# Performance work log

Hardware: AMD Instinct MI355X
Metric: run time of the kernel (lower is better)

## Reference

```python
import jax, jax.numpy as jnp
import numpy as np

C = 32          # d_model / channels
D_STATE = 32
D_CONV = 4
EXPAND = 2
D_INNER = EXPAND * C          # 64
DT_RANK = (C + 15) // 16      # ceil(32/16) = 2
EPS = 1e-5


def _conv2d(x, w, b):
    # x: (B,C,H,W), w: (O,I,3,3), stride 1, padding 1 (torch Conv2d)
    y = jax.lax.conv_general_dilated(
        x, w, window_strides=(1, 1), padding=[(1, 1), (1, 1)],
        dimension_numbers=("NCHW", "OIHW", "NCHW"))
    return y + b[None, :, None, None]


def _silu(x):
    return x * jax.nn.sigmoid(x)


def _mamba(xs, in_proj_w, conv1d_w, conv1d_b, x_proj_w, dt_proj_w, dt_proj_b,
           A_log, Dp, out_proj_w):
    # xs: (B, L, C)
    xz = xs @ in_proj_w.T                       # (B, L, 2*D_INNER)
    xm, z = jnp.split(xz, 2, axis=-1)           # each (B, L, D_INNER)

    # causal depthwise conv1d along L (torch: padding=d_conv-1 then [..., :L])
    xc = xm.transpose(0, 2, 1)                  # (B, D_INNER, L)
    xc = jax.lax.conv_general_dilated(
        xc, conv1d_w, window_strides=(1,), padding=[(D_CONV - 1, 0)],
        dimension_numbers=("NCH", "OIH", "NCH"),
        feature_group_count=D_INNER)
    xm = _silu((xc + conv1d_b[None, :, None]).transpose(0, 2, 1))  # (B,L,D_INNER)

    x_dbl = xm @ x_proj_w.T                     # (B, L, DT_RANK + 2*D_STATE)
    dt = x_dbl[..., :DT_RANK]
    Bm = x_dbl[..., DT_RANK:DT_RANK + D_STATE]  # (B, L, N)
    Cm = x_dbl[..., DT_RANK + D_STATE:]         # (B, L, N)

    delta = jax.nn.softplus(dt @ dt_proj_w.T + dt_proj_b)  # (B, L, D_INNER)
    A = -jnp.exp(A_log)                                     # (D_INNER, N)

    deltaA = jnp.exp(delta[..., None] * A)                           # (B,L,D,N)
    deltaBx = delta[..., None] * Bm[:, :, None, :] * xm[..., None]   # (B,L,D,N)

    def combine(c1, c2):
        a1, b1 = c1
        a2, b2 = c2
        return a1 * a2, a2 * b1 + b2

    # parallel linear recurrence h_t = deltaA_t * h_{t-1} + deltaBx_t
    _, hstate = jax.lax.associative_scan(combine, (deltaA, deltaBx), axis=1)

    y = jnp.einsum("bldn,bln->bld", hstate, Cm) + xm * Dp
    y = y * _silu(z)
    return y @ out_proj_w.T                     # (B, L, C)


def setup_inputs() -> dict:
    key = jax.random.key(0)
    ks = jax.random.split(key, 16)
    s = 0.02
    inp = {
        "x": jax.random.normal(ks[0], (4, C, 64, 64), dtype=jnp.float32),
        "conv1_w": jax.random.normal(ks[1], (2 * C, C, 3, 3), jnp.float32) * s,
        "conv1_b": jnp.zeros((2 * C,), jnp.float32),
        "conv2_w": jax.random.normal(ks[2], (C, 2 * C, 3, 3), jnp.float32) * s,
        "conv2_b": jnp.zeros((C,), jnp.float32),
        "ln_g": jnp.ones((C,), jnp.float32),
        "ln_b": jnp.zeros((C,), jnp.float32),
        "in_proj_w": jax.random.normal(ks[3], (2 * D_INNER, C), jnp.float32) * s,
        "conv1d_w": jax.random.normal(ks[4], (D_INNER, 1, D_CONV), jnp.float32) * 0.1,
        "conv1d_b": jnp.zeros((D_INNER,), jnp.float32),
        "x_proj_w": jax.random.normal(ks[5], (DT_RANK + 2 * D_STATE, D_INNER), jnp.float32) * s,
        "dt_proj_w": jax.random.normal(ks[6], (D_INNER, DT_RANK), jnp.float32) * 0.1,
        "dt_proj_b": jax.random.normal(ks[7], (D_INNER,), jnp.float32) * 0.1 - 4.0,
        "A_log": jnp.log(jnp.tile(jnp.arange(1, D_STATE + 1, dtype=jnp.float32), (D_INNER, 1))),
        "Dp": jnp.ones((D_INNER,), jnp.float32),
        "out_proj_w": jax.random.normal(ks[8], (C, D_INNER), jnp.float32) * s,
        "smooth_w": jax.random.normal(ks[9], (C, C, 3, 3), jnp.float32) * s,
        "smooth_b": jnp.zeros((C,), jnp.float32),
    }
    return inp


def reference(x, conv1_w, conv1_b, conv2_w, conv2_b, ln_g, ln_b,
              in_proj_w, conv1d_w, conv1d_b, x_proj_w, dt_proj_w, dt_proj_b,
              A_log, Dp, out_proj_w, smooth_w, smooth_b):
    b, c, h, w = x.shape
    # convb residual
    t = jax.nn.relu(_conv2d(x, conv1_w, conv1_b))
    x = _conv2d(t, conv2_w, conv2_b) + x
    # reshape (b,c,h,w) -> (b, h*w, c) row-major (faithful to torch .reshape)
    xs = x.reshape(b, -1, c)
    # LayerNorm over last dim
    mu = jnp.mean(xs, axis=-1, keepdims=True)
    var = jnp.mean(jnp.square(xs - mu), axis=-1, keepdims=True)
    xs = (xs - mu) * jax.lax.rsqrt(var + EPS) * ln_g + ln_b
    # Mamba block
    y = _mamba(xs, in_proj_w, conv1d_w, conv1d_b, x_proj_w, dt_proj_w,
               dt_proj_b, A_log, Dp, out_proj_w)
    y = y.transpose(0, 2, 1).reshape(b, c, h, w)
    return _conv2d(y, smooth_w, smooth_b)
```

## Files before the change

### kernel.cpp

```cpp
#include <hip/hip_runtime.h>
#include <math.h>

#define SEQL 4096
#define L2E 1.44269504088896340736f

#if defined(__has_builtin)
#if __has_builtin(__builtin_amdgcn_exp2f)
#define FAST_EXP2(x) __builtin_amdgcn_exp2f(x)
#endif
#endif
#ifndef FAST_EXP2
#define FAST_EXP2(x) exp2f(x)
#endif

__device__ __forceinline__ float sigmoid_f(float x){ return 1.0f/(1.0f+expf(-x)); }

template<int CI, int CO, int COG, bool RELU, bool RES>
__global__ __launch_bounds__(256) void conv3x3_k(const float* __restrict__ in,
    const float* __restrict__ wgt, const float* __restrict__ bias,
    const float* __restrict__ res, float* __restrict__ out)
{
  constexpr int CIT = CI/4;
  __shared__ float tin[4][2][6][72];
  __shared__ float red[3][4][COG][66];
  const int tid  = threadIdx.x;
  const int lane = tid & 63;
  const int ty   = tid >> 6;
  const int h0   = blockIdx.x * 4;
  const int co0  = blockIdx.y * COG;
  const int b    = blockIdx.z;

  if (lane < 24){
    int cl = lane / 12, rem = lane % 12, r = rem >> 1, side = rem & 1;
    tin[ty][cl][r][side ? 68 : 3] = 0.0f;
  }

  float acc[4][COG];
  #pragma unroll
  for (int rr=0;rr<4;++rr)
    #pragma unroll
    for (int u=0;u<COG;++u) acc[rr][u] = 0.0f;

  const int ci0 = ty*CIT;
  for (int cig = ci0; cig < ci0 + CIT; cig += 2){
    #pragma unroll
    for (int k=0;k<3;++k){
      int idx4 = lane + (k<<6);
      int row  = idx4 >> 4;
      int cl = row/6, r = row - cl*6;
      int w4 = (idx4 & 15) << 2;
      int h  = h0 - 1 + r;
      float4 v = make_float4(0.f,0.f,0.f,0.f);
      if (h>=0 && h<64)
        v = *(const float4*)(in + ((size_t)(b*CI+cig+cl)*64 + h)*64 + w4);
      *(float4*)&tin[ty][cl][r][4+w4] = v;
    }
    #pragma unroll
    for (int cl=0; cl<2; ++cl){
      float rv[6][3];
      #pragma unroll
      for (int r=0;r<6;++r)
        #pragma unroll
        for (int c=0;c<3;++c)
          rv[r][c] = tin[ty][cl][r][3+lane+c];
      #pragma unroll
      for (int u=0;u<COG;++u){
        const float* wp = wgt + ((size_t)(co0+u)*CI + cig + cl)*9;
        #pragma unroll
        for (int rr=0;rr<4;++rr)
          #pragma unroll
          for (int j=0;j<3;++j){
            acc[rr][u] = fmaf(rv[rr+j][0], wp[3*j+0], acc[rr][u]);
            acc[rr][u] = fmaf(rv[rr+j][1], wp[3*j+1], acc[rr][u]);
            acc[rr][u] = fmaf(rv[rr+j][2], wp[3*j+2], acc[rr][u]);
          }
      }
    }
  }
  if (ty > 0){
    #pragma unroll
    for (int rr=0;rr<4;++rr)
      #pragma unroll
      for (int u=0;u<COG;++u) red[ty-1][rr][u][lane] = acc[rr][u];
  }
  __syncthreads();
  if (ty == 0){
    #pragma unroll
    for (int rr=0;rr<4;++rr)
      #pragma unroll
      for (int u=0;u<COG;++u){
        float s = acc[rr][u] + red[0][rr][u][lane] + red[1][rr][u][lane]
                + red[2][rr][u][lane] + bias[co0+u];
        size_t ob = ((size_t)(b*CO+co0+u)*64 + h0+rr)*64 + lane;
        if constexpr (RES)  s += res[ob];
        if constexpr (RELU) s = fmaxf(s, 0.0f);
        out[ob] = s;
      }
  }
}

__global__ __launch_bounds__(512) void mamba_in_k(const float* __restrict__ x2,
    const float* __restrict__ g, const float* __restrict__ be,
    const float* __restrict__ Wip, const float* __restrict__ cw,
    const float* __restrict__ cb, const float* __restrict__ Wxp,
    const float* __restrict__ Wdt, const float* __restrict__ bdt,
    const float* __restrict__ A_log,
    float* __restrict__ xm2, float* __restrict__ szb, float* __restrict__ dlt,
    float* __restrict__ Bm, float* __restrict__ Cm,
    float* __restrict__ cA, float* __restrict__ cH)
{
  __shared__ float xn[35][37];
  __shared__ float xm[64][36];
  __shared__ float xt[32][67];
  __shared__ float xd[32][67];
  const int tid = threadIdx.x;
  const int bi = blockIdx.x >> 7;
  const int chunk = blockIdx.x & 127;
  const int l0 = chunk << 5;

  if (tid < 35){
    int tok = l0 - 3 + tid;
    if (tok >= 0){
      const float* row = x2 + (size_t)bi*131072 + (size_t)tok*32;
      float v[32];
      #pragma unroll
      for (int c=0;c<32;c+=4){
        float4 f = *(const float4*)(row + c);
        v[c]=f.x; v[c+1]=f.y; v[c+2]=f.z; v[c+3]=f.w;
      }
      float p[8];
      #pragma unroll
      for (int j2=0;j2<8;++j2) p[j2]=v[j2];
      #pragma unroll
      for (int i=8;i<32;i+=8){
        #pragma unroll
        for (int j2=0;j2<8;++j2) p[j2]+=v[i+j2];
      }
      float mu = (((p[0]+p[1])+(p[2]+p[3]))+((p[4]+p[5])+(p[6]+p[7]))) * 0.03125f;
      float q[8];
      #pragma unroll
      for (int j2=0;j2<8;++j2){ float dd=v[j2]-mu; q[j2]=dd*dd; }
      #pragma unroll
      for (int i=8;i<32;i+=8){
        #pragma unroll
        for (int j2=0;j2<8;++j2){ float dd=v[i+j2]-mu; q[j2]+=dd*dd; }
      }
      float var = (((q[0]+q[1])+(q[2]+q[3]))+((q[4]+q[5])+(q[6]+q[7]))) * 0.03125f;
      float rstd = 1.0f / sqrtf(var + 1e-5f);
      #pragma unroll
      for (int c=0;c<32;++c) xn[tid][c] = (v[c]-mu)*rstd*g[c] + be[c];
    } else {
      #pragma unroll
      for (int c=0;c<32;++c) xn[tid][c] = 0.0f;
    }
  }
  __syncthreads();

  {
    const int t = tid & 31, jg = tid >> 5;
    float xv[32];
    #pragma unroll
    for (int c=0;c<32;++c) xv[c] = xn[t+3][c];
    #pragma unroll
    for (int k=0;k<8;++k){
      int j = jg*8 + k;
      const float* wr = Wip + j*32;
      float a = 0.0f;
      #pragma unroll
      for (int c=0;c<32;++c) a = fmaf(xv[c], wr[c], a);
      if (j < 64) xm[j][t+3] = a;
      else        szb[((size_t)(bi*64 + (j-64)))*SEQL + l0 + t] = a * sigmoid_f(a);
    }
  }
  if (tid < 192){
    int t = tid % 3, j = tid / 3;
    float xv[32];
    #pragma unroll
    for (int c=0;c<32;++c) xv[c] = xn[t][c];
    const float* wr = Wip + j*32;
    float a = 0.0f;
    #pragma unroll
    for (int c=0;c<32;++c) a = fmaf(xv[c], wr[c], a);
    xm[j][t] = a;
  }
  __syncthreads();

  {
    const int d = tid >> 3, t0 = (tid & 7) << 2;
    const float w0=cw[d*4], w1=cw[d*4+1], w2=cw[d*4+2], w3=cw[d*4+3], bv=cb[d];
    float r[4];
    #pragma unroll
    for (int k=0;k<4;++k){
      int t = t0 + k;
      float a = xm[d][t]*w0 + xm[d][t+1]*w1 + xm[d][t+2]*w2 + xm[d][t+3]*w3 + bv;
      float s = a * sigmoid_f(a);
      xt[t][d] = s;
      r[k] = s;
    }
    *(float4*)(xm2 + ((size_t)(bi*64+d))*SEQL + l0 + t0) = make_float4(r[0],r[1],r[2],r[3]);
  }
  __syncthreads();

  {
    const int tok = tid & 31, jg = tid >> 5;
    float xv[64];
    #pragma unroll
    for (int c=0;c<64;++c) xv[c] = xt[tok][c];
    for (int j=jg; j<66; j+=16){
      const float* wr = Wxp + j*64;
      float a = 0.0f;
      #pragma unroll
      for (int c=0;c<64;++c) a = fmaf(xv[c], wr[c], a);
      xd[tok][j] = a;
    }
  }
  __syncthreads();

  {
    const int tok = tid & 31, gg = tid >> 5;
    float dt0 = xd[tok][0], dt1 = xd[tok][1];
    #pragma unroll
    for (int k=0;k<4;++k){
      int d2 = gg*4 + k;
      float v = dt0*Wdt[d2*2] + dt1*Wdt[d2*2+1] + bdt[d2];
      float sp = fmaxf(v,0.0f) + log1pf(expf(-fabsf(v)));
      dlt[((size_t)(bi*64+d2))*SEQL + l0 + tok] = sp;
      xm[d2][tok] = sp;
    }
    const int which = gg >> 3, n0 = (gg & 7)*4;
    float* dst = which ? Cm : Bm;
    const int s0 = 2 + which*32 + n0;
    float4 f;
    f.x = xd[tok][s0]; f.y = xd[tok][s0+1]; f.z = xd[tok][s0+2]; f.w = xd[tok][s0+3];
    *(float4*)(dst + ((size_t)bi*SEQL + l0 + tok)*32 + n0) = f;
  }
  __syncthreads();

  {
    const int d  = tid >> 3;
    const int gg = tid & 7;
    const int bd = bi*64 + d;
    float Av2[4], h[4] = {0,0,0,0}, aP[4] = {1,1,1,1};
    #pragma unroll
    for (int j=0;j<4;++j) Av2[j] = -expf(A_log[d*32 + gg + 8*j]) * L2E;
    #pragma unroll 4
    for (int t=0;t<32;++t){
      float dlv = xm[d][t];
      float xv2 = xt[t][d];
      #pragma unroll
      for (int j=0;j<4;++j){
        float bv = xd[t][2 + gg + 8*j];
        float a = FAST_EXP2(dlv*Av2[j]);
        h[j] = fmaf(a, h[j], dlv*bv*xv2);
        aP[j] *= a;
      }
    }
    #pragma unroll
    for (int j=0;j<4;++j){
      size_t idx = (((size_t)bd<<5) + gg + 8*j)*128 + chunk;
      cA[idx] = aP[j]; cH[idx] = h[j];
    }
  }
}

__global__ __launch_bounds__(256) void scan_p2(const float* __restrict__ dlt,
    const float* __restrict__ xssm, const float* __restrict__ Bm,
    const float* __restrict__ Cm, const float* __restrict__ A_log,
    const float* __restrict__ Dp, const float* __restrict__ sz,
    const float* __restrict__ cA, const float* __restrict__ cHs,
    float* __restrict__ yt)
{
  __shared__ float pre[32][9];
  const int tid = threadIdx.x;
  const int n = tid & 31;
  const int grp = blockIdx.x & 15;
  const int chunk = grp*8 + (tid >> 5);
  const int bd = blockIdx.x >> 4;
  const int b = bd >> 6, d = bd & 63;
  const int l0 = chunk << 5;

  if (tid < 32){
    const float* pa = cA  + (((size_t)bd<<5)+tid)*128;
    const float* ph = cHs + (((size_t)bd<<5)+tid)*128;
    float hrun = 0.0f;
    for (int c=0;c<grp*8;c+=4){
      float4 a4 = *(const float4*)(pa+c);
      float4 h4 = *(const float4*)(ph+c);
      hrun = fmaf(a4.x,hrun,h4.x);
      hrun = fmaf(a4.y,hrun,h4.y);
      hrun = fmaf(a4.z,hrun,h4.z);
      hrun = fmaf(a4.w,hrun,h4.w);
    }
    int c = grp*8;
    float4 a4 = *(const float4*)(pa+c);
    float4 h4 = *(const float4*)(ph+c);
    pre[tid][0]=hrun; hrun=fmaf(a4.x,hrun,h4.x);
    pre[tid][1]=hrun; hrun=fmaf(a4.y,hrun,h4.y);
    pre[tid][2]=hrun; hrun=fmaf(a4.z,hrun,h4.z);
    pre[tid][3]=hrun; hrun=fmaf(a4.w,hrun,h4.w);
    a4 = *(const float4*)(pa+c+4);
    h4 = *(const float4*)(ph+c+4);
    pre[tid][4]=hrun; hrun=fmaf(a4.x,hrun,h4.x);
    pre[tid][5]=hrun; hrun=fmaf(a4.y,hrun,h4.y);
    pre[tid][6]=hrun; hrun=fmaf(a4.z,hrun,h4.z);
    pre[tid][7]=hrun;
  }
  __syncthreads();

  const float Av2 = -expf(A_log[d*32+n]) * L2E;
  const float Dv = Dp[d];
  const float* del = dlt  + (size_t)bd*SEQL + l0;
  const float* xp  = xssm + (size_t)bd*SEQL + l0;
  const float* szp = sz   + (size_t)bd*SEQL + l0;
  const float* Bp  = Bm + ((size_t)b*SEQL + l0)*32 + n;
  const float* Cp  = Cm + ((size_t)b*SEQL + l0)*32 + n;
  float* yp = yt + (size_t)bd*SEQL + l0;
  float h = pre[n][tid >> 5];
  #pragma unroll 2
  for (int i0=0;i0<32;i0+=4){
    float4 d4 = *(const float4*)(del+i0);
    float4 x4 = *(const float4*)(xp +i0);
    float4 s4 = *(const float4*)(szp+i0);
    float b0 = Bp[(i0+0)*32], b1 = Bp[(i0+1)*32], b2 = Bp[(i0+2)*32], b3 = Bp[(i0+3)*32];
    float c0 = Cp[(i0+0)*32], c1 = Cp[(i0+1)*32], c2 = Cp[(i0+2)*32], c3 = Cp[(i0+3)*32];
    float a0 = FAST_EXP2(d4.x*Av2); h = fmaf(a0,h, d4.x*b0*x4.x);
    float v0 = h*c0;
    float a1 = FAST_EXP2(d4.y*Av2); h = fmaf(a1,h, d4.y*b1*x4.y);
    float v1 = h*c1;
    float a2 = FAST_EXP2(d4.z*Av2); h = fmaf(a2,h, d4.z*b2*x4.z);
    float v2 = h*c2;
    float a3 = FAST_EXP2(d4.w*Av2); h = fmaf(a3,h, d4.w*b3*x4.w);
    float v3 = h*c3;
    v0 += __shfl_xor(v0,16); v0 += __shfl_xor(v0,8); v0 += __shfl_xor(v0,4);
    v0 += __shfl_xor(v0,2);  v0 += __shfl_xor(v0,1);
    v1 += __shfl_xor(v1,16); v1 += __shfl_xor(v1,8); v1 += __shfl_xor(v1,4);
    v1 += __shfl_xor(v1,2);  v1 += __shfl_xor(v1,1);
    v2 += __shfl_xor(v2,16); v2 += __shfl_xor(v2,8); v2 += __shfl_xor(v2,4);
    v2 += __shfl_xor(v2,2);  v2 += __shfl_xor(v2,1);
    v3 += __shfl_xor(v3,16); v3 += __shfl_xor(v3,8); v3 += __shfl_xor(v3,4);
    v3 += __shfl_xor(v3,2);  v3 += __shfl_xor(v3,1);
    if (n==0){
      yp[i0+0] = fmaf(x4.x, Dv, v0) * s4.x;
      yp[i0+1] = fmaf(x4.y, Dv, v1) * s4.y;
      yp[i0+2] = fmaf(x4.z, Dv, v2) * s4.z;
      yp[i0+3] = fmaf(x4.w, Dv, v3) * s4.w;
    }
  }
}

__global__ __launch_bounds__(512) void outproj_k(const float* __restrict__ yt,
    const float* __restrict__ Wout, float* __restrict__ ym)
{
  __shared__ float ys[64][67];
  const int tid = threadIdx.x, lane = tid & 63, ty = tid >> 6;
  const int bi = blockIdx.x >> 6;
  const int l0 = (blockIdx.x & 63) << 6;
  for (int r=ty; r<64; r+=8)
    ys[lane][r] = yt[((size_t)(bi*64+r))*SEQL + l0 + lane];
  __syncthreads();
  float yv[64];
  #pragma unroll
  for (int c=0;c<64;++c) yv[c] = ys[lane][c];
  #pragma unroll
  for (int jj=0;jj<4;++jj){
    int j = ty*4 + jj;
    const float* wr = Wout + j*64;
    float acc = 0.0f;
    #pragma unroll
    for (int c=0;c<64;++c) acc = fmaf(yv[c], wr[c], acc);
    ym[((size_t)(bi*32+j))*SEQL + l0 + lane] = acc;
  }
}

extern "C" void kernel_launch(void* const* d_in, const int* in_sizes, int n_in,
                              void* d_out, int out_size, void* d_ws, size_t ws_size,
                              hipStream_t stream) {
  const float* x        = (const float*)d_in[0];
  const float* conv1_w  = (const float*)d_in[1];
  const float* conv1_b  = (const float*)d_in[2];
  const float* conv2_w  = (const float*)d_in[3];
  const float* conv2_b  = (const float*)d_in[4];
  const float* ln_g     = (const float*)d_in[5];
  const float* ln_b     = (const float*)d_in[6];
  const float* in_proj_w= (const float*)d_in[7];
  const float* conv1d_w = (const float*)d_in[8];
  const float* conv1d_b = (const float*)d_in[9];
  const float* x_proj_w = (const float*)d_in[10];
  const float* dt_proj_w= (const float*)d_in[11];
  const float* dt_proj_b= (const float*)d_in[12];
  const float* A_log    = (const float*)d_in[13];
  const float* Dp       = (const float*)d_in[14];
  const float* out_proj_w=(const float*)d_in[15];
  const float* smooth_w = (const float*)d_in[16];
  const float* smooth_b = (const float*)d_in[17];
  float* out = (float*)d_out;

  float* ws = (float*)d_ws;
  float* t      = ws;
  float* x2     = t      + 1048576;
  float* xm2    = x2     + 524288;
  float* szb    = xm2    + 1048576;
  float* dlt    = szb    + 1048576;
  float* Bmat   = dlt    + 1048576;
  float* Cmat   = Bmat   + 524288;
  float* yt     = Cmat   + 524288;
  float* ym     = yt     + 1048576;
  float* cA     = ym     + 524288;
  float* cH     = cA     + 1048576;

  conv3x3_k<32,64,4,true ,false><<<dim3(16,16,4), 256, 0, stream>>>(x,  conv1_w, conv1_b, nullptr, t);
  conv3x3_k<64,32,4,false,true ><<<dim3(16,8,4), 256, 0, stream>>>(t,  conv2_w, conv2_b, x,       x2);
  mamba_in_k  <<<512, 512, 0, stream>>>(x2, ln_g, ln_b, in_proj_w, conv1d_w, conv1d_b,
                                        x_proj_w, dt_proj_w, dt_proj_b, A_log,
                                        xm2, szb, dlt, Bmat, Cmat, cA, cH);
  scan_p2     <<<4096, 256, 0, stream>>>(dlt, xm2, Bmat, Cmat, A_log, Dp, szb, cA, cH, yt);
  outproj_k   <<<256, 512, 0, stream>>>(yt, out_proj_w, ym);
  conv3x3_k<32,32,4,false,false><<<dim3(16,8,4), 256, 0, stream>>>(ym, smooth_w, smooth_b, nullptr, out);
}
```

Baseline: 234.8 us.

## Give each scan thread four states and interleave B/C layout for float4 loads

The second scan pass now assigns 8 threads per 32-token chunk, each holding 4 of the 32 SSM states, instead of one thread per state. The B and C matrices are stored interleaved by state group so each thread can fetch its four values with one float4 load. The per-token reduction shrinks from a 5-step to a 3-step shuffle, the output is written as float4, and the grid shrinks fourfold. The carry prefix now walks 32 chunks serially per block, which lengthens the single-thread prologue.

```diff
diff --git a/kernel.cpp b/kernel.cpp
--- a/kernel.cpp
+++ b/kernel.cpp
@@ -227,12 +227,13 @@
       dlt[((size_t)(bi*64+d2))*SEQL + l0 + tok] = sp;
       xm[d2][tok] = sp;
     }
-    const int which = gg >> 3, n0 = (gg & 7)*4;
+    const int which = gg >> 3, qq = gg & 7;
     float* dst = which ? Cm : Bm;
-    const int s0 = 2 + which*32 + n0;
+    const int s2 = 2 + which*32;
     float4 f;
-    f.x = xd[tok][s0]; f.y = xd[tok][s0+1]; f.z = xd[tok][s0+2]; f.w = xd[tok][s0+3];
-    *(float4*)(dst + ((size_t)bi*SEQL + l0 + tok)*32 + n0) = f;
+    f.x = xd[tok][s2+qq+ 0]; f.y = xd[tok][s2+qq+ 8];
+    f.z = xd[tok][s2+qq+16]; f.w = xd[tok][s2+qq+24];
+    *(float4*)(dst + ((size_t)bi*SEQL + l0 + tok)*32 + qq*4) = f;
   }
   __syncthreads();
 
@@ -270,20 +271,18 @@
     const float* __restrict__ cA, const float* __restrict__ cHs,
     float* __restrict__ yt)
 {
-  __shared__ float pre[32][9];
+  __shared__ float pre[32][34];
   const int tid = threadIdx.x;
-  const int n = tid & 31;
-  const int grp = blockIdx.x & 15;
-  const int chunk = grp*8 + (tid >> 5);
-  const int bd = blockIdx.x >> 4;
+  const int grp = blockIdx.x & 3;
+  const int bd  = blockIdx.x >> 2;
   const int b = bd >> 6, d = bd & 63;
-  const int l0 = chunk << 5;
+  const int c0 = grp << 5;
 
   if (tid < 32){
     const float* pa = cA  + (((size_t)bd<<5)+tid)*128;
     const float* ph = cHs + (((size_t)bd<<5)+tid)*128;
     float hrun = 0.0f;
-    for (int c=0;c<grp*8;c+=4){
+    for (int c=0;c<c0;c+=4){
       float4 a4 = *(const float4*)(pa+c);
       float4 h4 = *(const float4*)(ph+c);
       hrun = fmaf(a4.x,hrun,h4.x);
@@ -291,60 +290,58 @@
       hrun = fmaf(a4.z,hrun,h4.z);
       hrun = fmaf(a4.w,hrun,h4.w);
     }
-    int c = grp*8;
-    float4 a4 = *(const float4*)(pa+c);
-    float4 h4 = *(const float4*)(ph+c);
-    pre[tid][0]=hrun; hrun=fmaf(a4.x,hrun,h4.x);
-    pre[tid][1]=hrun; hrun=fmaf(a4.y,hrun,h4.y);
-    pre[tid][2]=hrun; hrun=fmaf(a4.z,hrun,h4.z);
-    pre[tid][3]=hrun; hrun=fmaf(a4.w,hrun,h4.w);
-    a4 = *(const float4*)(pa+c+4);
-    h4 = *(const float4*)(ph+c+4);
-    pre[tid][4]=hrun; hrun=fmaf(a4.x,hrun,h4.x);
-    pre[tid][5]=hrun; hrun=fmaf(a4.y,hrun,h4.y);
-    pre[tid][6]=hrun; hrun=fmaf(a4.z,hrun,h4.z);
-    pre[tid][7]=hrun;
-  }
-  __syncthreads();
-
-  const float Av2 = -expf(A_log[d*32+n]) * L2E;
+    #pragma unroll 4
+    for (int k=0;k<32;k+=4){
+      float4 a4 = *(const float4*)(pa+c0+k);
+      float4 h4 = *(const float4*)(ph+c0+k);
+      pre[tid][k+0]=hrun; hrun=fmaf(a4.x,hrun,h4.x);
+      pre[tid][k+1]=hrun; hrun=fmaf(a4.y,hrun,h4.y);
+      pre[tid][k+2]=hrun; hrun=fmaf(a4.z,hrun,h4.z);
+      pre[tid][k+3]=hrun; hrun=fmaf(a4.w,hrun,h4.w);
+    }
+  }
+  __syncthreads();
+
+  const int lc = tid >> 3, gg = tid & 7;
+  const int chunk = c0 + lc;
+  const int l0 = chunk << 5;
   const float Dv = Dp[d];
+  float Av2[4], h[4];
+  #pragma unroll
+  for (int j=0;j<4;++j){
+    Av2[j] = -expf(A_log[d*32 + gg + 8*j]) * L2E;
+    h[j] = pre[gg + 8*j][lc];
+  }
   const float* del = dlt  + (size_t)bd*SEQL + l0;
   const float* xp  = xssm + (size_t)bd*SEQL + l0;
   const float* szp = sz   + (size_t)bd*SEQL + l0;
-  const float* Bp  = Bm + ((size_t)b*SEQL + l0)*32 + n;
-  const float* Cp  = Cm + ((size_t)b*SEQL + l0)*32 + n;
+  const float* Bp  = Bm + ((size_t)b*SEQL + l0)*32 + gg*4;
+  const float* Cp  = Cm + ((size_t)b*SEQL + l0)*32 + gg*4;
   float* yp = yt + (size_t)bd*SEQL + l0;
-  float h = pre[n][tid >> 5];
+
   #pragma unroll 2
   for (int i0=0;i0<32;i0+=4){
     float4 d4 = *(const float4*)(del+i0);
     float4 x4 = *(const float4*)(xp +i0);
     float4 s4 = *(const float4*)(szp+i0);
-    float b0 = Bp[(i0+0)*32], b1 = Bp[(i0+1)*32], b2 = Bp[(i0+2)*32], b3 = Bp[(i0+3)*32];
-    float c0 = Cp[(i0+0)*32], c1 = Cp[(i0+1)*32], c2 = Cp[(i0+2)*32], c3 = Cp[(i0+3)*32];
-    float a0 = FAST_EXP2(d4.x*Av2); h = fmaf(a0,h, d4.x*b0*x4.x);
-    float v0 = h*c0;
-    float a1 = FAST_EXP2(d4.y*Av2); h = fmaf(a1,h, d4.y*b1*x4.y);
-    float v1 = h*c1;
-    float a2 = FAST_EXP2(d4.z*Av2); h = fmaf(a2,h, d4.z*b2*x4.z);
-    float v2 = h*c2;
-    float a3 = FAST_EXP2(d4.w*Av2); h = fmaf(a3,h, d4.w*b3*x4.w);
-    float v3 = h*c3;
-    v0 += __shfl_xor(v0,16); v0 += __shfl_xor(v0,8); v0 += __shfl_xor(v0,4);
-    v0 += __shfl_xor(v0,2);  v0 += __shfl_xor(v0,1);
-    v1 += __shfl_xor(v1,16); v1 += __shfl_xor(v1,8); v1 += __shfl_xor(v1,4);
-    v1 += __shfl_xor(v1,2);  v1 += __shfl_xor(v1,1);
-    v2 += __shfl_xor(v2,16); v2 += __shfl_xor(v2,8); v2 += __shfl_xor(v2,4);
-    v2 += __shfl_xor(v2,2);  v2 += __shfl_xor(v2,1);
-    v3 += __shfl_xor(v3,16); v3 += __shfl_xor(v3,8); v3 += __shfl_xor(v3,4);
-    v3 += __shfl_xor(v3,2);  v3 += __shfl_xor(v3,1);
-    if (n==0){
-      yp[i0+0] = fmaf(x4.x, Dv, v0) * s4.x;
-      yp[i0+1] = fmaf(x4.y, Dv, v1) * s4.y;
-      yp[i0+2] = fmaf(x4.z, Dv, v2) * s4.z;
-      yp[i0+3] = fmaf(x4.w, Dv, v3) * s4.w;
-    }
+    float y[4];
+    #pragma unroll
+    for (int t=0;t<4;++t){
+      float dl = (t==0)? d4.x : (t==1)? d4.y : (t==2)? d4.z : d4.w;
+      float xl = (t==0)? x4.x : (t==1)? x4.y : (t==2)? x4.z : x4.w;
+      float sl = (t==0)? s4.x : (t==1)? s4.y : (t==2)? s4.z : s4.w;
+      float4 bv = *(const float4*)(Bp + (i0+t)*32);
+      float4 cv = *(const float4*)(Cp + (i0+t)*32);
+      float a0 = FAST_EXP2(dl*Av2[0]); h[0] = fmaf(a0, h[0], dl*bv.x*xl);
+      float a1 = FAST_EXP2(dl*Av2[1]); h[1] = fmaf(a1, h[1], dl*bv.y*xl);
+      float a2 = FAST_EXP2(dl*Av2[2]); h[2] = fmaf(a2, h[2], dl*bv.z*xl);
+      float a3 = FAST_EXP2(dl*Av2[3]); h[3] = fmaf(a3, h[3], dl*bv.w*xl);
+      float v = fmaf(h[3], cv.w, fmaf(h[2], cv.z, fmaf(h[1], cv.y, h[0]*cv.x)));
+      v += __shfl_xor(v,1); v += __shfl_xor(v,2); v += __shfl_xor(v,4);
+      y[t] = fmaf(xl, Dv, v) * sl;
+    }
+    if (gg == 0)
+      *(float4*)(yp + i0) = make_float4(y[0], y[1], y[2], y[3]);
   }
 }
 
@@ -413,7 +410,7 @@
   mamba_in_k  <<<512, 512, 0, stream>>>(x2, ln_g, ln_b, in_proj_w, conv1d_w, conv1d_b,
                                         x_proj_w, dt_proj_w, dt_proj_b, A_log,
                                         xm2, szb, dlt, Bmat, Cmat, cA, cH);
-  scan_p2     <<<4096, 256, 0, stream>>>(dlt, xm2, Bmat, Cmat, A_log, Dp, szb, cA, cH, yt);
+  scan_p2     <<<1024, 256, 0, stream>>>(dlt, xm2, Bmat, Cmat, A_log, Dp, szb, cA, cH, yt);
   outproj_k   <<<256, 512, 0, stream>>>(yt, out_proj_w, ym);
   conv3x3_k<32,32,4,false,false><<<dim3(16,8,4), 256, 0, stream>>>(ym, smooth_w, smooth_b, nullptr, out);
 }
```

Result: faster. 207.9 us (-11.4%).
